# Kernel tuning notes

Measured on AMD Instinct MI355X. Metric: run time of the kernel, lower is better.

## Reference

```python
import jax, jax.numpy as jnp
import numpy as np

D_MODEL = 1024
NUM_HEADS = 16
DEPTH = D_MODEL // NUM_HEADS


def setup_inputs() -> dict:
    key = jax.random.key(0)
    ks = jax.random.split(key, 9)
    B, S = 2, 2048
    scale = 1.0 / np.sqrt(D_MODEL)
    x = jax.random.normal(ks[0], (B, S, D_MODEL), dtype=jnp.float32)
    wq = jax.random.normal(ks[1], (D_MODEL, D_MODEL), dtype=jnp.float32) * scale
    bq = jax.random.normal(ks[2], (D_MODEL,), dtype=jnp.float32) * 0.01
    wk = jax.random.normal(ks[3], (D_MODEL, D_MODEL), dtype=jnp.float32) * scale
    bk = jax.random.normal(ks[4], (D_MODEL,), dtype=jnp.float32) * 0.01
    wv = jax.random.normal(ks[5], (D_MODEL, D_MODEL), dtype=jnp.float32) * scale
    bv = jax.random.normal(ks[6], (D_MODEL,), dtype=jnp.float32) * 0.01
    wo = jax.random.normal(ks[7], (D_MODEL, D_MODEL), dtype=jnp.float32) * scale
    bo = jax.random.normal(ks[8], (D_MODEL,), dtype=jnp.float32) * 0.01
    return {"x": x, "wq": wq, "bq": bq, "wk": wk, "bk": bk,
            "wv": wv, "bv": bv, "wo": wo, "bo": bo}


def reference(x, wq, bq, wk, bk, wv, bv, wo, bo):
    B, S, _ = x.shape
    def split_heads(t):  # [B,S,D] -> [B,H,S,depth]
        return t.reshape(B, S, NUM_HEADS, DEPTH).transpose(0, 2, 1, 3)
    q = split_heads(x @ wq + bq)
    k = split_heads(x @ wk + bk)
    v = split_heads(x @ wv + bv)
    # scaled dot-product attention, full [B,H,S,S] scores as in the original
    logits = jnp.einsum('bhqd,bhkd->bhqk', q, k) / jnp.sqrt(
        jnp.asarray(DEPTH, dtype=jnp.float32))
    attn = jax.nn.softmax(logits, axis=-1)
    out = jnp.einsum('bhqk,bhkd->bhqd', attn, v)
    out = out.transpose(0, 2, 1, 3).reshape(B, S, D_MODEL)
    return out @ wo + bo
```

## Files before the change

kernel.cpp:

```cpp
#include <hip/hip_runtime.h>


#define S_LEN 2048
#define DM 1024
#define MROWS 4096
#define QSCALE 0.1803368801111244f

typedef unsigned short u16;
typedef unsigned int u32;
typedef __attribute__((ext_vector_type(8))) short short8;
typedef __attribute__((ext_vector_type(4))) float f32x4;
typedef __attribute__((ext_vector_type(4))) unsigned short u16x4;
typedef __attribute__((ext_vector_type(2))) unsigned int u32x2;

__device__ inline u16 f2bf(float f) {
    u32 u = __float_as_uint(f);
    u = u + 0x7fffu + ((u >> 16) & 1u);
    return (u16)(u >> 16);
}
__device__ inline void gld_lds16(const u16* g, u16* l) {
    __builtin_amdgcn_global_load_lds(
        (const __attribute__((address_space(1))) void*)g,
        (__attribute__((address_space(3))) void*)l, 16, 0, 0);
}
__device__ inline f32x4 mfma16(short8 a, short8 b, f32x4 c) {
    return __builtin_amdgcn_mfma_f32_16x16x32_bf16(a, b, c, 0, 0, 0);
}

__global__ void prep_all(const float* __restrict__ x, u16* __restrict__ xb,
                         const float* __restrict__ wq, const float* __restrict__ wk,
                         const float* __restrict__ wv, const float* __restrict__ wo,
                         const float* __restrict__ bq, const float* __restrict__ bk,
                         const float* __restrict__ bv, const float* __restrict__ bo,
                         u16* __restrict__ wallT, u16* __restrict__ woT,
                         float* __restrict__ biasAll, float* __restrict__ biasO) {
    const int t = threadIdx.x;
    if (blockIdx.x < 2048) {
        const size_t i8 = ((size_t)blockIdx.x * 256 + t) * 8;
        const f32x4 a = ((const f32x4*)x)[i8 / 4];
        const f32x4 b = ((const f32x4*)x)[i8 / 4 + 1];
        u16 o[8];
#pragma unroll
        for (int i = 0; i < 4; i++) { o[i] = f2bf(a[i]); o[4 + i] = f2bf(b[i]); }
        *(short8*)(xb + i8) = *(const short8*)o;
        return;
    }
    const int bid = blockIdx.x - 2048;
    if (bid == 1024) {
#pragma unroll
        for (int i = 0; i < 4; i++) {
            const int idx = i * 256 + t;
            biasAll[idx]        = bq[idx] * QSCALE;
            biasAll[1024 + idx] = bk[idx];
            biasAll[2048 + idx] = bv[idx];
            biasO[idx]          = bo[idx];
        }
        return;
    }
    __shared__ float lds[64][65];
    const int m  = bid >> 8;
    const int tk = (bid >> 4) & 15;
    const int tn = bid & 15;
    const float* src = (m == 0) ? wq : (m == 1) ? wk : (m == 2) ? wv : wo;
    const float scale = (m == 0) ? QSCALE : 1.0f;
    const int r4 = t >> 6, c = t & 63;
#pragma unroll
    for (int i = 0; i < 16; i++) {
        const int k = tk * 64 + i * 4 + r4;
        lds[i * 4 + r4][c] = src[(size_t)k * 1024 + tn * 64 + c];
    }
    __syncthreads();
#pragma unroll
    for (int i = 0; i < 16; i++) {
        const int n = tn * 64 + i * 4 + r4;
        const int k = tk * 64 + c;
        const u16 v = f2bf(lds[c][i * 4 + r4] * scale);
        if (m < 3) wallT[((size_t)m * 1024 + n) * 1024 + k] = v;
        else       woT[(size_t)n * 1024 + k] = v;
    }
}

__global__ __launch_bounds__(256, 2)
void gemm_qkv(const u16* __restrict__ A, const u16* __restrict__ Bt,
              const float* __restrict__ bias, u16* __restrict__ Cq,
              u16* __restrict__ Ck, u16* __restrict__ Cv,
              const int K, const int N) {
    __shared__ __align__(16) u16 As[128 * 32];
    __shared__ __align__(16) u16 Bs[128 * 32];
    __shared__ __align__(16) u16 Ct[128 * 136];
    const int tid = threadIdx.x;
    const int w = tid >> 6, lane = tid & 63;
    const int wm = w >> 1, wn = w & 1;
    const int l16 = lane & 15, quad = lane >> 4;
    const int tm = blockIdx.x * 128;
    const int tn = blockIdx.y * 128;
    const int region = tn >> 10;

    const int sr = w * 16 + (lane >> 2);
    const int sc = (lane & 3) * 8;
    const u16* ag0 = A + (size_t)(tm + sr) * K + sc;
    const u16* ag1 = A + (size_t)(tm + sr + 64) * K + sc;
    const u16* bg0 = Bt + (size_t)(tn + sr) * K + sc;
    const u16* bg1 = Bt + (size_t)(tn + sr + 64) * K + sc;
    u16* al = As + w * 512;
    u16* bl = Bs + w * 512;

    f32x4 acc[4][4];
#pragma unroll
    for (int i = 0; i < 4; i++)
#pragma unroll
        for (int j = 0; j < 4; j++) acc[i][j] = (f32x4){0.f, 0.f, 0.f, 0.f};

    for (int kb = 0; kb < K; kb += 32) {
        __syncthreads();
        gld_lds16(ag0 + kb, al);
        gld_lds16(ag1 + kb, al + 2048);
        gld_lds16(bg0 + kb, bl);
        gld_lds16(bg1 + kb, bl + 2048);
        __syncthreads();
        short8 af[4], bfr[4];
#pragma unroll
        for (int i = 0; i < 4; i++) {
            af[i]  = *(const short8*)(As + (wm * 64 + i * 16 + l16) * 32 + quad * 8);
            bfr[i] = *(const short8*)(Bs + (wn * 64 + i * 16 + l16) * 32 + quad * 8);
        }
#pragma unroll
        for (int i = 0; i < 4; i++)
#pragma unroll
            for (int j = 0; j < 4; j++)
                acc[i][j] = mfma16(af[i], bfr[j], acc[i][j]);
    }

    if (region < 2) {
#pragma unroll
        for (int j = 0; j < 4; j++) {
            const int colL = wn * 64 + j * 16 + l16;
            const float bv = bias[tn + colL];
#pragma unroll
            for (int i = 0; i < 4; i++) {
                const int row0 = wm * 64 + i * 16 + quad * 4;
#pragma unroll
                for (int r = 0; r < 4; r++)
                    Ct[(row0 + r) * 136 + colL] = f2bf(acc[i][j][r] + bv);
            }
        }
    } else {
#pragma unroll
        for (int j = 0; j < 4; j++) {
            const int colL = wn * 64 + j * 16 + l16;
            const float bv = bias[tn + colL];
#pragma unroll
            for (int i = 0; i < 4; i++) {
                const int row0 = wm * 64 + i * 16 + quad * 4;
                u16x4 pk;
#pragma unroll
                for (int r = 0; r < 4; r++) pk[r] = f2bf(acc[i][j][r] + bv);
                *(u16x4*)(Ct + colL * 132 + row0) = pk;
            }
        }
    }
    __syncthreads();

    if (region == 0) {
#pragma unroll
        for (int p = 0; p < 8; p++) {
            const int rowL = p * 16 + (tid >> 4);
            const int c8 = (tid & 15) * 8;
            const short8 v = *(const short8*)(Ct + rowL * 136 + c8);
            *(short8*)(Cq + (size_t)(tm + rowL) * 1024 + tn + c8) = v;
        }
    } else if (region == 1) {
        const int b = tm >> 11, sBase = tm & 2047;
#pragma unroll
        for (int p = 0; p < 8; p++) {
            const int rowL = p * 16 + (tid >> 4);
            const int c8 = (tid & 15) * 8;
            const short8 v = *(const short8*)(Ct + rowL * 136 + c8);
            const int s = sBase + rowL;
            const int hd = (tn - 1024) + c8;
            const int h = hd >> 6, dd = hd & 63;
            const int chunk = ((dd >> 3) + s) & 7;
            *(short8*)(Ck + (((size_t)(b * 16 + h) * 2048 + s) << 6) + chunk * 8) = v;
        }
    } else {
        const int b = tm >> 11, tBase = (tm & 2047) >> 6;
        const int hBase = (tn >> 6) - 32;
#pragma unroll
        for (int p = 0; p < 8; p++) {
            const int cid = p * 256 + tid;
            const int q3 = cid & 7;
            const int colL = (cid >> 3) & 127;
            const int half = cid >> 10;
            const int d = colL & 63;
            const int h = hBase + (colL >> 6);
            const int c = (q3 - d) & 7;
            const int base = (c & 3) * 4 + ((c & 4) << 3);
            const u32x2 Ar = *(const u32x2*)(Ct + colL * 132 + half * 64 + base);
            const u32x2 Br = *(const u32x2*)(Ct + colL * 132 + half * 64 + base + 16);
            union { u32 u[4]; short8 s8; } o;
            o.u[0] = __builtin_amdgcn_perm(Br[0], Ar[0], 0x05040100u);
            o.u[1] = __builtin_amdgcn_perm(Br[0], Ar[0], 0x07060302u);
            o.u[2] = __builtin_amdgcn_perm(Br[1], Ar[1], 0x05040100u);
            o.u[3] = __builtin_amdgcn_perm(Br[1], Ar[1], 0x07060302u);
            *(short8*)(Cv + (((size_t)((b * 16 + h) * 32 + tBase + half)) << 12) +
                       d * 64 + q3 * 8) = o.s8;
        }
    }
}

__global__ __launch_bounds__(256, 2)
void gemm_out64(const u16* __restrict__ A, const u16* __restrict__ Bt,
                const float* __restrict__ bias, float* __restrict__ C,
                const int K, const int N) {
    __shared__ __align__(16) u16 As[64 * 32];
    __shared__ __align__(16) u16 Bs[128 * 32];
    const int tid = threadIdx.x;
    const int w = tid >> 6, lane = tid & 63;
    const int wm = w >> 1, wn = w & 1;
    const int l16 = lane & 15, quad = lane >> 4;
    const int tm = blockIdx.x * 64;
    const int tn = blockIdx.y * 128;

    const int sr = w * 16 + (lane >> 2);
    const int sc = (lane & 3) * 8;
    const u16* ag  = A + (size_t)(tm + sr) * K + sc;
    const u16* bg0 = Bt + (size_t)(tn + sr) * K + sc;
    const u16* bg1 = Bt + (size_t)(tn + sr + 64) * K + sc;
    u16* al = As + w * 512;
    u16* bl = Bs + w * 512;

    f32x4 acc[2][4];
#pragma unroll
    for (int i = 0; i < 2; i++)
#pragma unroll
        for (int j = 0; j < 4; j++) acc[i][j] = (f32x4){0.f, 0.f, 0.f, 0.f};

    for (int kb = 0; kb < K; kb += 32) {
        __syncthreads();
        gld_lds16(ag + kb, al);
        gld_lds16(bg0 + kb, bl);
        gld_lds16(bg1 + kb, bl + 2048);
        __syncthreads();
        short8 af[2], bfr[4];
#pragma unroll
        for (int i = 0; i < 2; i++)
            af[i] = *(const short8*)(As + (wm * 32 + i * 16 + l16) * 32 + quad * 8);
#pragma unroll
        for (int j = 0; j < 4; j++)
            bfr[j] = *(const short8*)(Bs + (wn * 64 + j * 16 + l16) * 32 + quad * 8);
#pragma unroll
        for (int i = 0; i < 2; i++)
#pragma unroll
            for (int j = 0; j < 4; j++)
                acc[i][j] = mfma16(af[i], bfr[j], acc[i][j]);
    }
#pragma unroll
    for (int j = 0; j < 4; j++) {
        const int col = tn + wn * 64 + j * 16 + l16;
        const float bv = bias[col];
#pragma unroll
        for (int i = 0; i < 2; i++) {
            const int row0 = tm + wm * 32 + i * 16 + quad * 4;
#pragma unroll
            for (int r = 0; r < 4; r++)
                C[(size_t)(row0 + r) * N + col] = acc[i][j][r] + bv;
        }
    }
}

__global__ __launch_bounds__(256, 2)
void flash_attn(const u16* __restrict__ Qb, const u16* __restrict__ Ktg,
                const u16* __restrict__ Vtb, u16* __restrict__ O) {
    __shared__ __align__(16) u16 Ks[4096];
    __shared__ __align__(16) u16 Vs[4096];
    const int tid = threadIdx.x;
    const int w = tid >> 6, lane = tid & 63;
    const int l16 = lane & 15, quad = lane >> 4;
    const int bh = blockIdx.y, b = bh >> 4, h = bh & 15;
    const int q0 = blockIdx.x * 128 + w * 32;

    short8 qf[2][2];
#pragma unroll
    for (int u = 0; u < 2; u++) {
        const size_t qrow = (size_t)(b * S_LEN + q0 + u * 16 + l16) * 1024 + h * 64;
        qf[u][0] = *(const short8*)(Qb + qrow + quad * 8);
        qf[u][1] = *(const short8*)(Qb + qrow + 32 + quad * 8);
    }
    u16 ones_s[8];
#pragma unroll
    for (int i = 0; i < 8; i++) ones_s[i] = 0x3F80u;
    const short8 ones = *(const short8*)ones_s;

    const u16* kg = Ktg + ((size_t)bh << 17) + w * 1024 + lane * 8;
    const u16* vg = Vtb + ((size_t)bh << 17) + w * 1024 + lane * 8;
    u16* kl = Ks + w * 1024;
    u16* vl = Vs + w * 1024;

    const int ka0 = l16 * 64 + ((quad + l16) & 7) * 8;
    const int ka1 = l16 * 64 + ((4 + quad + l16) & 7) * 8;

    f32x4 o[2][4], osum[2];
#pragma unroll
    for (int u = 0; u < 2; u++) {
        osum[u] = (f32x4){0.f, 0.f, 0.f, 0.f};
#pragma unroll
        for (int d = 0; d < 4; d++) o[u][d] = (f32x4){0.f, 0.f, 0.f, 0.f};
    }
    const f32x4 zz = (f32x4){0.f, 0.f, 0.f, 0.f};

    for (int t = 0; t < S_LEN / 64; t++) {
        __syncthreads();
        const int off = t * 4096;
        gld_lds16(kg + off,       kl);
        gld_lds16(kg + off + 512, kl + 512);
        gld_lds16(vg + off,       vl);
        gld_lds16(vg + off + 512, vl + 512);
        __syncthreads();

        f32x4 s[2][4];
#pragma unroll
        for (int a = 0; a < 4; a++) {
            const short8 kf0 = *(const short8*)(Ks + a * 1024 + ka0);
            const short8 kf1 = *(const short8*)(Ks + a * 1024 + ka1);
#pragma unroll
            for (int u = 0; u < 2; u++) {
                s[u][a] = mfma16(kf0, qf[u][0], zz);
                s[u][a] = mfma16(kf1, qf[u][1], s[u][a]);
            }
        }
        union { u32 u[4]; short8 s8; } pu[2][2];
#pragma unroll
        for (int u = 0; u < 2; u++) {
#pragma unroll
            for (int r = 0; r < 4; r++) {
                const float e0 = __builtin_amdgcn_exp2f(s[u][0][r]);
                const float e1 = __builtin_amdgcn_exp2f(s[u][1][r]);
                const float e2 = __builtin_amdgcn_exp2f(s[u][2][r]);
                const float e3 = __builtin_amdgcn_exp2f(s[u][3][r]);
                pu[u][0].u[r] = __builtin_amdgcn_perm(
                    __float_as_uint(e1), __float_as_uint(e0), 0x07060302u);
                pu[u][1].u[r] = __builtin_amdgcn_perm(
                    __float_as_uint(e3), __float_as_uint(e2), 0x07060302u);
            }
            osum[u] = mfma16(ones, pu[u][0].s8, osum[u]);
            osum[u] = mfma16(ones, pu[u][1].s8, osum[u]);
        }
#pragma unroll
        for (int dv = 0; dv < 4; dv++) {
            const short8 vf0 = *(const short8*)(Vs + dv * 1024 + ka0);
            const short8 vf1 = *(const short8*)(Vs + dv * 1024 + ka1);
#pragma unroll
            for (int u = 0; u < 2; u++) {
                o[u][dv] = mfma16(vf0, pu[u][0].s8, o[u][dv]);
                o[u][dv] = mfma16(vf1, pu[u][1].s8, o[u][dv]);
            }
        }
    }

#pragma unroll
    for (int u = 0; u < 2; u++) {
        const float inv = 1.0f / osum[u][0];
        const size_t obase =
            (size_t)(b * S_LEN + q0 + u * 16 + l16) * DM + h * 64 + quad * 4;
#pragma unroll
        for (int d = 0; d < 4; d++) {
            u16x4 pk;
#pragma unroll
            for (int r = 0; r < 4; r++) pk[r] = f2bf(o[u][d][r] * inv);
            *(u16x4*)(O + obase + d * 16) = pk;
        }
    }
}

extern "C" void kernel_launch(void* const* d_in, const int* in_sizes, int n_in,
                              void* d_out, int out_size, void* d_ws, size_t ws_size,
                              hipStream_t stream) {
    const float* x  = (const float*)d_in[0];
    const float* wq = (const float*)d_in[1];
    const float* bq = (const float*)d_in[2];
    const float* wk = (const float*)d_in[3];
    const float* bk = (const float*)d_in[4];
    const float* wv = (const float*)d_in[5];
    const float* bv = (const float*)d_in[6];
    const float* wo = (const float*)d_in[7];
    const float* bo = (const float*)d_in[8];

    char* ws = (char*)d_ws;
    u16*   wallT   = (u16*)(ws + 64);
    u16*   woT     = (u16*)(ws + 6291520);
    float* biasAll = (float*)(ws + 8388672);
    float* biasO   = (float*)(ws + 8400960);
    u16*   xb      = (u16*)(ws + 8405056);
    u16*   Qb      = (u16*)(ws + 16793664);
    u16*   Ktg     = (u16*)(ws + 25182272);
    u16*   Vtb     = (u16*)(ws + 33570880);
    u16*   Obuf    = (u16*)(ws + 41959488);

    prep_all<<<3073, 256, 0, stream>>>(x, xb, wq, wk, wv, wo, bq, bk, bv, bo,
                                       wallT, woT, biasAll, biasO);
    gemm_qkv<<<dim3(32, 24), 256, 0, stream>>>(xb, wallT, biasAll,
                                               Qb, Ktg, Vtb, 1024, 3072);
    flash_attn<<<dim3(16, 32), 256, 0, stream>>>(Qb, Ktg, Vtb, Obuf);
    gemm_out64<<<dim3(64, 8), 256, 0, stream>>>(Obuf, woT, biasO,
                                                (float*)d_out, 1024, 1024);
}
```

Measured before the change: 181.4 us.

## Split KV range across wave pairs with per-wave private LDS tiles, merge at end

Restructures flash attention so each pair of waves shares 64 query rows and each wave covers half of the key sequence, using its own private LDS buffer for K/V tiles. This removes the two block-wide __syncthreads per KV tile and replaces them with waitcnt on per-wave async loads. Each wave now holds 64 query rows, so every K/V fragment read from LDS feeds four MFMA row groups instead of two. The partial outputs and row sums are combined through LDS in a final reduction. LDS use grows to 64KB plus extra, and register pressure rises with o[4][4], which may limit occupancy under launch_bounds(256,2).

```diff
diff --git a/kernel.cpp b/kernel.cpp
--- a/kernel.cpp
+++ b/kernel.cpp
@@ -271,17 +271,18 @@
 __global__ __launch_bounds__(256, 2)
 void flash_attn(const u16* __restrict__ Qb, const u16* __restrict__ Ktg,
                 const u16* __restrict__ Vtb, u16* __restrict__ O) {
-    __shared__ __align__(16) u16 Ks[4096];
-    __shared__ __align__(16) u16 Vs[4096];
+    __shared__ __align__(16) u16 SB[4][8192];
+    __shared__ float osumS[4][4][16];
     const int tid = threadIdx.x;
     const int w = tid >> 6, lane = tid & 63;
     const int l16 = lane & 15, quad = lane >> 4;
     const int bh = blockIdx.y, b = bh >> 4, h = bh & 15;
-    const int q0 = blockIdx.x * 128 + w * 32;
-
-    short8 qf[2][2];
-#pragma unroll
-    for (int u = 0; u < 2; u++) {
+    const int qg = w >> 1, kh = w & 1;
+    const int q0 = blockIdx.x * 128 + qg * 64;
+
+    short8 qf[4][2];
+#pragma unroll
+    for (int u = 0; u < 4; u++) {
         const size_t qrow = (size_t)(b * S_LEN + q0 + u * 16 + l16) * 1024 + h * 64;
         qf[u][0] = *(const short8*)(Qb + qrow + quad * 8);
         qf[u][1] = *(const short8*)(Qb + qrow + 32 + quad * 8);
@@ -291,46 +292,47 @@
     for (int i = 0; i < 8; i++) ones_s[i] = 0x3F80u;
     const short8 ones = *(const short8*)ones_s;
 
-    const u16* kg = Ktg + ((size_t)bh << 17) + w * 1024 + lane * 8;
-    const u16* vg = Vtb + ((size_t)bh << 17) + w * 1024 + lane * 8;
-    u16* kl = Ks + w * 1024;
-    u16* vl = Vs + w * 1024;
+    const u16* kg = Ktg + ((size_t)bh << 17) + ((size_t)kh << 16) + lane * 8;
+    const u16* vg = Vtb + ((size_t)bh << 17) + ((size_t)kh << 16) + lane * 8;
+    u16* kl = &SB[w][0];
+    u16* vl = &SB[w][4096];
 
     const int ka0 = l16 * 64 + ((quad + l16) & 7) * 8;
     const int ka1 = l16 * 64 + ((4 + quad + l16) & 7) * 8;
 
-    f32x4 o[2][4], osum[2];
-#pragma unroll
-    for (int u = 0; u < 2; u++) {
+    f32x4 o[4][4], osum[4];
+#pragma unroll
+    for (int u = 0; u < 4; u++) {
         osum[u] = (f32x4){0.f, 0.f, 0.f, 0.f};
 #pragma unroll
         for (int d = 0; d < 4; d++) o[u][d] = (f32x4){0.f, 0.f, 0.f, 0.f};
     }
     const f32x4 zz = (f32x4){0.f, 0.f, 0.f, 0.f};
 
-    for (int t = 0; t < S_LEN / 64; t++) {
-        __syncthreads();
+    for (int t = 0; t < 16; t++) {
+        __builtin_amdgcn_sched_barrier(0);
         const int off = t * 4096;
-        gld_lds16(kg + off,       kl);
-        gld_lds16(kg + off + 512, kl + 512);
-        gld_lds16(vg + off,       vl);
-        gld_lds16(vg + off + 512, vl + 512);
-        __syncthreads();
-
-        f32x4 s[2][4];
+#pragma unroll
+        for (int j = 0; j < 8; j++) gld_lds16(kg + off + j * 512, kl + j * 512);
+#pragma unroll
+        for (int j = 0; j < 8; j++) gld_lds16(vg + off + j * 512, vl + j * 512);
+        __builtin_amdgcn_s_waitcnt(0x0F70);
+        __builtin_amdgcn_sched_barrier(0);
+
+        f32x4 s[4][4];
 #pragma unroll
         for (int a = 0; a < 4; a++) {
-            const short8 kf0 = *(const short8*)(Ks + a * 1024 + ka0);
-            const short8 kf1 = *(const short8*)(Ks + a * 1024 + ka1);
-#pragma unroll
-            for (int u = 0; u < 2; u++) {
+            const short8 kf0 = *(const short8*)(kl + a * 1024 + ka0);
+            const short8 kf1 = *(const short8*)(kl + a * 1024 + ka1);
+#pragma unroll
+            for (int u = 0; u < 4; u++) {
                 s[u][a] = mfma16(kf0, qf[u][0], zz);
                 s[u][a] = mfma16(kf1, qf[u][1], s[u][a]);
             }
         }
-        union { u32 u[4]; short8 s8; } pu[2][2];
-#pragma unroll
-        for (int u = 0; u < 2; u++) {
+        union { u32 u[4]; short8 s8; } pu[4][2];
+#pragma unroll
+        for (int u = 0; u < 4; u++) {
 #pragma unroll
             for (int r = 0; r < 4; r++) {
                 const float e0 = __builtin_amdgcn_exp2f(s[u][0][r]);
@@ -347,27 +349,41 @@
         }
 #pragma unroll
         for (int dv = 0; dv < 4; dv++) {
-            const short8 vf0 = *(const short8*)(Vs + dv * 1024 + ka0);
-            const short8 vf1 = *(const short8*)(Vs + dv * 1024 + ka1);
-#pragma unroll
-            for (int u = 0; u < 2; u++) {
+            const short8 vf0 = *(const short8*)(vl + dv * 1024 + ka0);
+            const short8 vf1 = *(const short8*)(vl + dv * 1024 + ka1);
+#pragma unroll
+            for (int u = 0; u < 4; u++) {
                 o[u][dv] = mfma16(vf0, pu[u][0].s8, o[u][dv]);
                 o[u][dv] = mfma16(vf1, pu[u][1].s8, o[u][dv]);
             }
         }
     }
 
-#pragma unroll
-    for (int u = 0; u < 2; u++) {
-        const float inv = 1.0f / osum[u][0];
-        const size_t obase =
-            (size_t)(b * S_LEN + q0 + u * 16 + l16) * DM + h * 64 + quad * 4;
-#pragma unroll
-        for (int d = 0; d < 4; d++) {
-            u16x4 pk;
-#pragma unroll
-            for (int r = 0; r < 4; r++) pk[r] = f2bf(o[u][d][r] * inv);
-            *(u16x4*)(O + obase + d * 16) = pk;
+    float* pb = (float*)&SB[w][0];
+#pragma unroll
+    for (int u = 0; u < 4; u++) {
+#pragma unroll
+        for (int dv = 0; dv < 4; dv++)
+            *(f32x4*)(pb + (u * 4 + dv) * 256 + lane * 4) = o[u][dv];
+        if (quad == 0) osumS[w][u][l16] = osum[u][0];
+    }
+    __syncthreads();
+    if (kh == 0) {
+        const float* qb2 = (const float*)&SB[w + 1][0];
+#pragma unroll
+        for (int u = 0; u < 4; u++) {
+            const float inv = 1.0f / (osumS[w][u][l16] + osumS[w + 1][u][l16]);
+            const size_t obase =
+                (size_t)(b * S_LEN + q0 + u * 16 + l16) * DM + h * 64 + quad * 4;
+#pragma unroll
+            for (int dv = 0; dv < 4; dv++) {
+                const f32x4 other = *(const f32x4*)(qb2 + (u * 4 + dv) * 256 + lane * 4);
+                u16x4 pk;
+#pragma unroll
+                for (int r = 0; r < 4; r++)
+                    pk[r] = f2bf((o[u][dv][r] + other[r]) * inv);
+                *(u16x4*)(O + obase + dv * 16) = pk;
+            }
         }
     }
 }
```

Result: no change. 183.6 us (+1.2%).
